# Kernel optimization log

Measured on AMD Instinct MI355X. Metric: run time of the kernel, lower is better.

The kernel has to match this reference:

```python
import jax, jax.numpy as jnp
from jax import lax
import numpy as np

B, C, FH, FW, H, V, L = 256, 512, 8, 16, 512, 64, 24


def setup_inputs() -> dict:
    key = jax.random.key(0)
    ks = jax.random.split(key, 32)
    s = 0.05
    n = lambda k, shp: jax.random.normal(k, shp, dtype=jnp.float32) * s
    return {
        "encoder_ftrs": jax.random.normal(ks[0], (B, C, FH, FW), dtype=jnp.float32),
        "sequences": jax.random.randint(ks[1], (B, L), 0, V),
        "test": 0,
        "embed_w": n(ks[2], (V, H)),
        "init_state": n(ks[3], (2, 1, H)),
        "attn_W_w": n(ks[4], (H, C)), "attn_W_b": jnp.zeros((H,), jnp.float32),
        "attn_U_w": n(ks[5], (H, H)), "attn_U_b": jnp.zeros((H,), jnp.float32),
        "attn_v_w": n(ks[6], (1, H)), "attn_v_b": jnp.zeros((1,), jnp.float32),
        "fc_w": n(ks[7], (H, C + H)), "fc_b": jnp.zeros((H,), jnp.float32),
        "cls_w": n(ks[8], (V, H)), "cls_b": jnp.zeros((V,), jnp.float32),
        "gru0_wih": n(ks[9], (3 * H, 2 * H)), "gru0_whh": n(ks[10], (3 * H, H)),
        "gru0_bih": jnp.zeros((3 * H,), jnp.float32), "gru0_bhh": jnp.zeros((3 * H,), jnp.float32),
        "gru1_wih": n(ks[11], (3 * H, H)), "gru1_whh": n(ks[12], (3 * H, H)),
        "gru1_bih": jnp.zeros((3 * H,), jnp.float32), "gru1_bhh": jnp.zeros((3 * H,), jnp.float32),
    }


def _gru_cell(x, h, wih, whh, bih, bhh):
    # PyTorch GRUCell: r,z gates then candidate n with r applied on hidden path
    gi = x @ wih.T + bih
    gh = h @ whh.T + bhh
    i_r, i_z, i_n = jnp.split(gi, 3, axis=-1)
    h_r, h_z, h_n = jnp.split(gh, 3, axis=-1)
    r = jax.nn.sigmoid(i_r + h_r)
    z = jax.nn.sigmoid(i_z + h_z)
    nact = jnp.tanh(i_n + r * h_n)
    return (1.0 - z) * nact + z * h


def reference(encoder_ftrs, sequences, test, embed_w, init_state,
              attn_W_w, attn_W_b, attn_U_w, attn_U_b, attn_v_w, attn_v_b,
              fc_w, fc_b, cls_w, cls_b,
              gru0_wih, gru0_whh, gru0_bih, gru0_bhh,
              gru1_wih, gru1_whh, gru1_bih, gru1_bhh):
    bsz = encoder_ftrs.shape[0]
    # [B, L_sp, C] encoder states
    states = encoder_ftrs.reshape(bsz, C, -1).transpose(0, 2, 1)
    # attn_W(states) is timestep-independent: precompute once (same math)
    Ws = states @ attn_W_w.T + attn_W_b  # [B, L_sp, H]

    def apply_attn(h_top):
        e = jax.nn.relu(Ws + (h_top @ attn_U_w.T + attn_U_b)[:, None, :])
        scores = e @ attn_v_w[0] + attn_v_b[0]          # [B, L_sp]
        a = jax.nn.softmax(scores, axis=-1)
        ctx = jnp.einsum('bl,blc->bc', a, states)        # [B, C]
        return ctx

    def out_proj(ctx, h_top):
        return jax.nn.relu(jnp.concatenate([ctx, h_top], axis=-1) @ fc_w.T + fc_b)

    xs = embed_w[sequences[:, :-1]]                      # [B, T, H]
    h0 = jnp.broadcast_to(init_state, (2, bsz, H))       # repeat over batch
    y0 = out_proj(apply_attn(h0[1]), h0[1])              # time_step == -1 (output dropped)

    def step(carry, x_t):
        h, y = carry
        h_l0 = _gru_cell(jnp.concatenate([y, x_t], axis=-1), h[0],
                         gru0_wih, gru0_whh, gru0_bih, gru0_bhh)
        h_l1 = _gru_cell(h_l0, h[1], gru1_wih, gru1_whh, gru1_bih, gru1_bhh)
        hn = jnp.stack([h_l0, h_l1], axis=0)
        yn = out_proj(apply_attn(h_l1), h_l1)
        return (hn, yn), yn

    _, ys = lax.scan(step, (h0, y0), xs.transpose(1, 0, 2))   # [T, B, H]
    logits = ys.transpose(1, 0, 2) @ cls_w.T + cls_b          # [B, T, V]

    labels = sequences[:, 1:]
    mask = (labels > 0).astype(logits.dtype)
    logp = jax.nn.log_softmax(logits, axis=-1)
    nll = -jnp.take_along_axis(logp, labels[..., None], axis=-1)[..., 0]
    loss = jnp.sum(nll * mask) / jnp.sum(mask)
    return loss
```

## Files before the change

kernel.cpp:

```cpp
#include <hip/hip_runtime.h>
#include <hip/hip_bf16.h>
#include <cstddef>

#define BB 256
#define CC 512
#define SS 128
#define HH 512
#define VV 64
#define LL 24

typedef unsigned short ush;
typedef __attribute__((ext_vector_type(8))) short short8;
typedef __attribute__((ext_vector_type(4))) float f32x4;

__device__ __forceinline__ float wave_sum(float v) {
#pragma unroll
    for (int off = 32; off > 0; off >>= 1) v += __shfl_xor(v, off);
    return v;
}
__device__ __forceinline__ float wave_max(float v) {
#pragma unroll
    for (int off = 32; off > 0; off >>= 1) v = fmaxf(v, __shfl_xor(v, off));
    return v;
}
__device__ __forceinline__ float sigm(float x) { return 1.0f / (1.0f + expf(-x)); }
__device__ __forceinline__ ush f2bf(float f) {
    unsigned u = __float_as_uint(f);
    u += 0x7FFFu + ((u >> 16) & 1u);
    return (ush)(u >> 16);
}
__device__ __forceinline__ float bf2f(ush b) {
    return __uint_as_float(((unsigned)b) << 16);
}
__device__ __forceinline__ unsigned pack2(float a, float b) {
    return (unsigned)f2bf(a) | ((unsigned)f2bf(b) << 16);
}

__global__ __launch_bounds__(256) void init_kernel(const float* __restrict__ init_state,
                                                   float* __restrict__ h0,
                                                   float* __restrict__ h1,
                                                   ush* __restrict__ h0b,
                                                   ush* __restrict__ h1b,
                                                   float* __restrict__ acc) {
    int idx = blockIdx.x * 256 + threadIdx.x;
    if (idx < BB * HH) {
        float a = init_state[idx & (HH - 1)];
        float b = init_state[HH + (idx & (HH - 1))];
        h0[idx] = a; h1[idx] = b;
        h0b[idx] = f2bf(a); h1b[idx] = f2bf(b);
    }
    if (idx < 2) acc[idx] = 0.0f;
}

__global__ __launch_bounds__(256) void conv_kernel(const float* __restrict__ src,
                                                   ush* __restrict__ dst, int n4) {
    int i = blockIdx.x * 256 + threadIdx.x;
    if (i < n4) {
        float4 v = ((const float4*)src)[i];
        uint2 o;
        o.x = pack2(v.x, v.y);
        o.y = pack2(v.z, v.w);
        ((uint2*)dst)[i] = o;
    }
}

__global__ __launch_bounds__(128) void gather_kernel(const float* __restrict__ embed_w,
                                                     const int* __restrict__ seq,
                                                     ush* __restrict__ xall) {
    int item = blockIdx.x;
    int t = item >> 8, m = item & 255;
    int row = seq[m * LL + t];
    float4 v = ((const float4*)(embed_w + (size_t)row * HH))[threadIdx.x];
    uint2 o;
    o.x = pack2(v.x, v.y);
    o.y = pack2(v.z, v.w);
    ((uint2*)(xall + (size_t)item * HH))[threadIdx.x] = o;
}

__global__ __launch_bounds__(256) void ws_mfma(const float* __restrict__ enc,
                                               const ush* __restrict__ Wb,
                                               const float* __restrict__ bias,
                                               ush* __restrict__ Ws_bf) {
    int tid = threadIdx.x;
    int wave = tid >> 6, lane = tid & 63;
    int quad = lane >> 4, l16 = lane & 15;
    int m0 = blockIdx.x * 256 + wave * 64;
    int n0 = blockIdx.y * 64;
    int b = m0 >> 7;
    int s_base = m0 & 127;
    const float* eb = enc + (size_t)b * CC * SS;
    const ush* wp = Wb + (size_t)(n0 + l16) * 512 + quad * 8;
    f32x4 acc[4][4];
#pragma unroll
    for (int f = 0; f < 4; f++)
#pragma unroll
        for (int s = 0; s < 4; s++) acc[f][s] = (f32x4){0.f, 0.f, 0.f, 0.f};
    for (int k0 = 0; k0 < 512; k0 += 32) {
        short8 af[4], bfr[4];
#pragma unroll
        for (int f = 0; f < 4; f++) {
            int s = s_base + f * 16 + l16;
#pragma unroll
            for (int j = 0; j < 8; j++) {
                float v = eb[(size_t)(k0 + quad * 8 + j) * SS + s];
                af[f][j] = (short)f2bf(v);
            }
        }
#pragma unroll
        for (int s = 0; s < 4; s++)
            bfr[s] = *(const short8*)(wp + (size_t)s * 16 * 512 + k0);
#pragma unroll
        for (int f = 0; f < 4; f++)
#pragma unroll
            for (int s = 0; s < 4; s++)
                acc[f][s] = __builtin_amdgcn_mfma_f32_16x16x32_bf16(af[f], bfr[s], acc[f][s], 0, 0, 0);
    }
#pragma unroll
    for (int f = 0; f < 4; f++)
#pragma unroll
        for (int s = 0; s < 4; s++)
#pragma unroll
            for (int r = 0; r < 4; r++) {
                int m = m0 + f * 16 + quad * 4 + r;
                int n = n0 + s * 16 + l16;
                Ws_bf[(size_t)m * HH + n] = f2bf(acc[f][s][r] + bias[n]);
            }
}

struct SkArgs {
    const ush* x[3];
    const ush* w[3];
    int wst[3];
};

__global__ __launch_bounds__(256) void mfma_gemm(SkArgs args, int N, int M,
                                                 float* __restrict__ P) {
    int tid = threadIdx.x;
    int wave = tid >> 6, lane = tid & 63;
    int quad = lane >> 4, l16 = lane & 15;
    int m0 = blockIdx.x * 64 + wave * 16;
    int n0 = blockIdx.y * 64;
    int z = blockIdx.z;
    const ush* X = args.x[z];
    const ush* W = args.w[z];
    int wst = args.wst[z];
    const ush* xp = X + (size_t)(m0 + l16) * 512 + quad * 8;
    const ush* wp = W + (size_t)(n0 + l16) * wst + quad * 8;
    f32x4 acc[4];
#pragma unroll
    for (int s = 0; s < 4; s++) acc[s] = (f32x4){0.f, 0.f, 0.f, 0.f};
    short8 a_c, b_c[4];
    a_c = *(const short8*)(xp);
#pragma unroll
    for (int s = 0; s < 4; s++) b_c[s] = *(const short8*)(wp + (size_t)s * 16 * wst);
#pragma unroll
    for (int ks = 0; ks < 16; ks++) {
        short8 a_n, b_n[4];
        if (ks < 15) {
            int k = (ks + 1) * 32;
            a_n = *(const short8*)(xp + k);
#pragma unroll
            for (int s = 0; s < 4; s++) b_n[s] = *(const short8*)(wp + (size_t)s * 16 * wst + k);
        }
#pragma unroll
        for (int s = 0; s < 4; s++)
            acc[s] = __builtin_amdgcn_mfma_f32_16x16x32_bf16(a_c, b_c[s], acc[s], 0, 0, 0);
        if (ks < 15) {
            a_c = a_n;
#pragma unroll
            for (int s = 0; s < 4; s++) b_c[s] = b_n[s];
        }
    }
#pragma unroll
    for (int s = 0; s < 4; s++)
#pragma unroll
        for (int r = 0; r < 4; r++) {
            int m = m0 + quad * 4 + r;
            int n = n0 + s * 16 + l16;
            P[((size_t)z * M + m) * N + n] = acc[s][r];
        }
}

template <int NSTEP>
__device__ __forceinline__ void segk(const ush* __restrict__ ap,
                                     const ush* __restrict__ bp,
                                     size_t wofs, f32x4& a0, f32x4& a1) {
    short8 as[4], bs0[4], bs1[4];
    constexpr int PRE = NSTEP < 4 ? NSTEP : 4;
#pragma unroll
    for (int i = 0; i < PRE; i++) {
        as[i]  = *(const short8*)(ap + 32 * i);
        bs0[i] = *(const short8*)(bp + 32 * i);
        bs1[i] = *(const short8*)(bp + wofs + 32 * i);
    }
#pragma unroll
    for (int i = 0; i < NSTEP; i++) {
        const int sl = i & 3;
        a0 = __builtin_amdgcn_mfma_f32_16x16x32_bf16(as[sl], bs0[sl], a0, 0, 0, 0);
        a1 = __builtin_amdgcn_mfma_f32_16x16x32_bf16(as[sl], bs1[sl], a1, 0, 0, 0);
        if (i + 4 < NSTEP) {
            as[sl]  = *(const short8*)(ap + 32 * (i + 4));
            bs0[sl] = *(const short8*)(bp + 32 * (i + 4));
            bs1[sl] = *(const short8*)(bp + wofs + 32 * (i + 4));
        }
    }
}

struct GruArgs {
    const ush* xs[4][3];
    const ush* wb[4][3];
    int wst[4][3];
    int nseg[4];
};

__global__ __launch_bounds__(256) void gru_fused(GruArgs A,
                                                 const float* __restrict__ h_prev,
                                                 const float* __restrict__ bih,
                                                 const float* __restrict__ bhh,
                                                 float* __restrict__ h_out,
                                                 ush* __restrict__ h_out_bf) {
    int tid = threadIdx.x;
    int wave = __builtin_amdgcn_readfirstlane(tid >> 6);
    int lane = tid & 63, quad = lane >> 4, l16 = lane & 15;
    int m0 = blockIdx.x * 16, n0 = blockIdx.y * 32;
    f32x4 acc0 = (f32x4){0.f, 0.f, 0.f, 0.f};
    f32x4 acc1 = (f32x4){0.f, 0.f, 0.f, 0.f};
    int ns = A.nseg[wave];
#pragma unroll
    for (int s = 0; s < 3; s++) {
        if (s < ns) {
            int wst = A.wst[wave][s];
            const ush* ap = A.xs[wave][s] + (size_t)(m0 + l16) * 512 + quad * 8;
            const ush* bp = A.wb[wave][s] + (size_t)(n0 + l16) * wst + quad * 8;
            segk<16>(ap, bp, (size_t)16 * wst, acc0, acc1);
        }
    }
    __shared__ float gbuf[4][16][32];
#pragma unroll
    for (int r = 0; r < 4; r++) {
        gbuf[wave][quad * 4 + r][l16]      = acc0[r];
        gbuf[wave][quad * 4 + r][16 + l16] = acc1[r];
    }
    __syncthreads();
#pragma unroll
    for (int e = 0; e < 2; e++) {
        int idx = e * 256 + tid;
        int mi = idx >> 5, ni = idx & 31;
        int n = n0 + ni;
        size_t off = (size_t)(m0 + mi) * HH + n;
        float r  = sigm(gbuf[0][mi][ni] + bih[n] + bhh[n]);
        float zf = sigm(gbuf[1][mi][ni] + bih[512 + n] + bhh[512 + n]);
        float na = tanhf(gbuf[2][mi][ni] + bih[1024 + n] +
                         r * (gbuf[3][mi][ni] + bhh[1024 + n]));
        float hp = h_prev[off];
        float ho = (1.0f - zf) * na + zf * hp;
        h_out[off] = ho;
        h_out_bf[off] = f2bf(ho);
    }
}

__global__ __launch_bounds__(256) void fc_fused(const ush* __restrict__ ctx,
                                                const ush* __restrict__ h,
                                                const ush* __restrict__ wFc,
                                                const float* __restrict__ bias,
                                                ush* __restrict__ y,
                                                ush* __restrict__ ys) {
    int tid = threadIdx.x;
    int wave = __builtin_amdgcn_readfirstlane(tid >> 6);
    int lane = tid & 63, quad = lane >> 4, l16 = lane & 15;
    int m0 = blockIdx.x * 16, n0 = blockIdx.y * 32;
    f32x4 acc0 = (f32x4){0.f, 0.f, 0.f, 0.f};
    f32x4 acc1 = (f32x4){0.f, 0.f, 0.f, 0.f};
    const ush* X = (wave < 2) ? ctx : h;
    int xco = (wave & 1) * 256;
    const ush* ap = X + (size_t)(m0 + l16) * 512 + xco + quad * 8;
    const ush* bp = wFc + (size_t)(n0 + l16) * 1024 + wave * 256 + quad * 8;
    segk<8>(ap, bp, (size_t)16 * 1024, acc0, acc1);
    __shared__ float gbuf[4][16][32];
#pragma unroll
    for (int r = 0; r < 4; r++) {
        gbuf[wave][quad * 4 + r][l16]      = acc0[r];
        gbuf[wave][quad * 4 + r][16 + l16] = acc1[r];
    }
    __syncthreads();
#pragma unroll
    for (int e = 0; e < 2; e++) {
        int idx = e * 256 + tid;
        int mi = idx >> 5, ni = idx & 31;
        int n = n0 + ni;
        float v = gbuf[0][mi][ni] + gbuf[1][mi][ni] + gbuf[2][mi][ni] +
                  gbuf[3][mi][ni] + bias[n];
        v = fmaxf(v, 0.0f);
        ush bb = f2bf(v);
        size_t off = (size_t)(m0 + mi) * HH + n;
        y[off] = bb;
        if (ys) ys[off] = bb;
    }
}

__global__ __launch_bounds__(256) void u_fused(const ush* __restrict__ h,
                                               const ush* __restrict__ wU,
                                               const float* __restrict__ Ub,
                                               float* __restrict__ Uo) {
    int tid = threadIdx.x;
    int wave = __builtin_amdgcn_readfirstlane(tid >> 6);
    int lane = tid & 63, quad = lane >> 4, l16 = lane & 15;
    int m0 = blockIdx.x * 16, n0 = blockIdx.y * 32;
    f32x4 acc0 = (f32x4){0.f, 0.f, 0.f, 0.f};
    f32x4 acc1 = (f32x4){0.f, 0.f, 0.f, 0.f};
    const ush* ap = h + (size_t)(m0 + l16) * 512 + wave * 128 + quad * 8;
    const ush* bp = wU + (size_t)(n0 + l16) * 512 + wave * 128 + quad * 8;
    segk<4>(ap, bp, (size_t)16 * 512, acc0, acc1);
    __shared__ float gbuf[4][16][32];
#pragma unroll
    for (int r = 0; r < 4; r++) {
        gbuf[wave][quad * 4 + r][l16]      = acc0[r];
        gbuf[wave][quad * 4 + r][16 + l16] = acc1[r];
    }
    __syncthreads();
#pragma unroll
    for (int e = 0; e < 2; e++) {
        int idx = e * 256 + tid;
        int mi = idx >> 5, ni = idx & 31;
        int n = n0 + ni;
        Uo[(size_t)(m0 + mi) * HH + n] = gbuf[0][mi][ni] + gbuf[1][mi][ni] +
                                         gbuf[2][mi][ni] + gbuf[3][mi][ni] + Ub[n];
    }
}

__global__ __launch_bounds__(256) void attn2(const float* __restrict__ u,
                                             const float* __restrict__ vw,
                                             const ush* __restrict__ Ws_bf,
                                             const ush* __restrict__ enc_bf,
                                             ush* __restrict__ ctx_bf) {
    int b = blockIdx.x;
    int tid = threadIdx.x;
    int wave = tid >> 6, lane = tid & 63;
    int hi = lane >> 4, li = lane & 15;
    __shared__ float a[SS];

    float ur[4][8], vr[4][8];
#pragma unroll
    for (int p = 0; p < 4; p++) {
        const float* up = u + (size_t)b * HH + p * 128 + li * 8;
        const float* vp = vw + p * 128 + li * 8;
        float4 u0 = *(const float4*)(up);
        float4 u1 = *(const float4*)(up + 4);
        float4 v0 = *(const float4*)(vp);
        float4 v1 = *(const float4*)(vp + 4);
        ur[p][0] = u0.x; ur[p][1] = u0.y; ur[p][2] = u0.z; ur[p][3] = u0.w;
        ur[p][4] = u1.x; ur[p][5] = u1.y; ur[p][6] = u1.z; ur[p][7] = u1.w;
        vr[p][0] = v0.x; vr[p][1] = v0.y; vr[p][2] = v0.z; vr[p][3] = v0.w;
        vr[p][4] = v1.x; vr[p][5] = v1.y; vr[p][6] = v1.z; vr[p][7] = v1.w;
    }
    const ush* wsb = Ws_bf + (size_t)b * SS * HH;
#pragma unroll
    for (int pass = 0; pass < 8; pass++) {
        int s = pass * 16 + wave * 4 + hi;
        float acc = 0.0f;
#pragma unroll
        for (int p = 0; p < 4; p++) {
            short8 rv = *(const short8*)(wsb + (size_t)s * HH + p * 128 + li * 8);
#pragma unroll
            for (int j = 0; j < 8; j++) {
                float e = bf2f((ush)rv[j]) + ur[p][j];
                acc += fmaxf(e, 0.0f) * vr[p][j];
            }
        }
#pragma unroll
        for (int off = 1; off < 16; off <<= 1) acc += __shfl_xor(acc, off);
        if (li == 0) a[s] = acc;
    }
    __syncthreads();
    if (wave == 0) {
        float s0v = a[lane], s1v = a[lane + 64];
        float m = wave_max(fmaxf(s0v, s1v));
        float e0 = expf(s0v - m), e1 = expf(s1v - m);
        float ssum = wave_sum(e0 + e1);
        float inv = 1.0f / ssum;
        a[lane] = e0 * inv;
        a[lane + 64] = e1 * inv;
    }
    __syncthreads();
    float ar[8];
#pragma unroll
    for (int j = 0; j < 8; j++) ar[j] = a[li * 8 + j];
    const ush* eb = enc_bf + (size_t)b * CC * SS;
#pragma unroll 4
    for (int pass = 0; pass < 32; pass++) {
        int c = pass * 16 + wave * 4 + hi;
        short8 ev = *(const short8*)(eb + (size_t)c * SS + li * 8);
        float acc = 0.0f;
#pragma unroll
        for (int j = 0; j < 8; j++) acc += bf2f((ush)ev[j]) * ar[j];
#pragma unroll
        for (int off = 1; off < 16; off <<= 1) acc += __shfl_xor(acc, off);
        if (li == 0) ctx_bf[(size_t)b * CC + c] = f2bf(acc);
    }
}

__global__ __launch_bounds__(64) void nll_kernel(const float* __restrict__ P,
                                                 const float* __restrict__ cls_b,
                                                 const int* __restrict__ seq,
                                                 float* __restrict__ acc) {
    int lane = threadIdx.x;
    float bias = cls_b[lane];
    float lsum = 0.0f, lcnt = 0.0f;
    for (int i = 0; i < 16; i++) {
        int item = blockIdx.x * 16 + i;
        int t = item >> 8, b = item & 255;
        float v = P[(size_t)item * VV + lane] + bias;
        float m = wave_max(v);
        float e = expf(v - m);
        float s = wave_sum(e);
        int label = seq[b * LL + t + 1];
        float vl = __shfl(v, label);
        if (lane == 0 && label > 0) {
            lsum += -(vl - m - logf(s));
            lcnt += 1.0f;
        }
    }
    if (lane == 0) {
        atomicAdd(&acc[0], lsum);
        atomicAdd(&acc[1], lcnt);
    }
}

__global__ void final_kernel(const float* __restrict__ acc, float* __restrict__ out) {
    if (threadIdx.x == 0) out[0] = acc[0] / acc[1];
}

extern "C" void kernel_launch(void* const* d_in, const int* in_sizes, int n_in,
                              void* d_out, int out_size, void* d_ws, size_t ws_size,
                              hipStream_t stream) {
    const float* enc        = (const float*)d_in[0];
    const int*   seq        = (const int*)d_in[1];
    const float* embed_w    = (const float*)d_in[3];
    const float* init_state = (const float*)d_in[4];
    const float* attn_W_w   = (const float*)d_in[5];
    const float* attn_W_b   = (const float*)d_in[6];
    const float* attn_U_w   = (const float*)d_in[7];
    const float* attn_U_b   = (const float*)d_in[8];
    const float* attn_v_w   = (const float*)d_in[9];
    const float* fc_w       = (const float*)d_in[11];
    const float* fc_b       = (const float*)d_in[12];
    const float* cls_w      = (const float*)d_in[13];
    const float* cls_b      = (const float*)d_in[14];
    const float* g0_wih     = (const float*)d_in[15];
    const float* g0_whh     = (const float*)d_in[16];
    const float* g0_bih     = (const float*)d_in[17];
    const float* g0_bhh     = (const float*)d_in[18];
    const float* g1_wih     = (const float*)d_in[19];
    const float* g1_whh     = (const float*)d_in[20];
    const float* g1_bih     = (const float*)d_in[21];
    const float* g1_bhh     = (const float*)d_in[22];
    float* out = (float*)d_out;

    float* ws = (float*)d_ws;
    size_t o = 0;
    ush* Ws_bf   = (ush*)(ws + o); o += (size_t)BB * SS * HH / 2;
    ush* enc_bf  = (ush*)(ws + o); o += (size_t)BB * CC * SS / 2;
    ush* ys_bf   = (ush*)(ws + o); o += (size_t)(LL - 1) * BB * HH / 2;
    ush* xall_bf = (ush*)(ws + o); o += (size_t)(LL - 1) * BB * HH / 2;
    ush* wWb  = (ush*)(ws + o); o += 262144 / 2;
    ush* wU   = (ush*)(ws + o); o += 262144 / 2;
    ush* wFc  = (ush*)(ws + o); o += 524288 / 2;
    ush* wCls = (ush*)(ws + o); o += 32768 / 2;
    ush* wG0i = (ush*)(ws + o); o += 1572864 / 2;
    ush* wG0h = (ush*)(ws + o); o += 786432 / 2;
    ush* wG1i = (ush*)(ws + o); o += 786432 / 2;
    ush* wG1h = (ush*)(ws + o); o += 786432 / 2;
    float* P    = ws + o; o += (size_t)3 * BB * 1536;
    float* Uo   = ws + o; o += (size_t)BB * HH;
    float* h0a  = ws + o; o += (size_t)BB * HH;
    float* h0b  = ws + o; o += (size_t)BB * HH;
    float* h1a  = ws + o; o += (size_t)BB * HH;
    float* h1b  = ws + o; o += (size_t)BB * HH;
    float* acc  = ws + o; o += 256;
    ush* h0a_bf = (ush*)(ws + o); o += (size_t)BB * HH / 2;
    ush* h0b_bf = (ush*)(ws + o); o += (size_t)BB * HH / 2;
    ush* h1a_bf = (ush*)(ws + o); o += (size_t)BB * HH / 2;
    ush* h1b_bf = (ush*)(ws + o); o += (size_t)BB * HH / 2;
    ush* y_bf   = (ush*)(ws + o); o += (size_t)BB * HH / 2;
    ush* ctx_bf = (ush*)(ws + o); o += (size_t)BB * CC / 2;
    float* Pcls = P;

    init_kernel<<<512, 256, 0, stream>>>(init_state, h0a, h1a, h0a_bf, h1a_bf, acc);
    conv_kernel<<<256, 256, 0, stream>>>(attn_W_w, wWb, 65536);
    conv_kernel<<<256, 256, 0, stream>>>(attn_U_w, wU, 65536);
    conv_kernel<<<512, 256, 0, stream>>>(fc_w, wFc, 131072);
    conv_kernel<<<32, 256, 0, stream>>>(cls_w, wCls, 8192);
    conv_kernel<<<1536, 256, 0, stream>>>(g0_wih, wG0i, 393216);
    conv_kernel<<<768, 256, 0, stream>>>(g0_whh, wG0h, 196608);
    conv_kernel<<<768, 256, 0, stream>>>(g1_wih, wG1i, 196608);
    conv_kernel<<<768, 256, 0, stream>>>(g1_whh, wG1h, 196608);
    conv_kernel<<<16384, 256, 0, stream>>>(enc, enc_bf, 4194304);
    gather_kernel<<<(LL - 1) * BB, 128, 0, stream>>>(embed_w, seq, xall_bf);
    ws_mfma<<<dim3(128, 8), 256, 0, stream>>>(enc, wWb, attn_W_b, Ws_bf);

    auto gru0_args = [&](const ush* y, const ush* x, const ush* h0) {
        GruArgs a{};
        a.xs[0][0] = y;  a.wb[0][0] = wG0i;                          a.wst[0][0] = 1024;
        a.xs[0][1] = x;  a.wb[0][1] = wG0i + 512;                    a.wst[0][1] = 1024;
        a.xs[0][2] = h0; a.wb[0][2] = wG0h;                          a.wst[0][2] = 512;
        a.nseg[0] = 3;
        a.xs[1][0] = y;  a.wb[1][0] = wG0i + (size_t)512 * 1024;        a.wst[1][0] = 1024;
        a.xs[1][1] = x;  a.wb[1][1] = wG0i + (size_t)512 * 1024 + 512;  a.wst[1][1] = 1024;
        a.xs[1][2] = h0; a.wb[1][2] = wG0h + (size_t)512 * 512;         a.wst[1][2] = 512;
        a.nseg[1] = 3;
        a.xs[2][0] = y;  a.wb[2][0] = wG0i + (size_t)1024 * 1024;       a.wst[2][0] = 1024;
        a.xs[2][1] = x;  a.wb[2][1] = wG0i + (size_t)1024 * 1024 + 512; a.wst[2][1] = 1024;
        a.nseg[2] = 2;
        a.xs[3][0] = h0; a.wb[3][0] = wG0h + (size_t)1024 * 512;        a.wst[3][0] = 512;
        a.nseg[3] = 1;
        return a;
    };
    auto gru1_args = [&](const ush* hl0, const ush* h1) {
        GruArgs a{};
        a.xs[0][0] = hl0; a.wb[0][0] = wG1i;                        a.wst[0][0] = 512;
        a.xs[0][1] = h1;  a.wb[0][1] = wG1h;                        a.wst[0][1] = 512;
        a.nseg[0] = 2;
        a.xs[1][0] = hl0; a.wb[1][0] = wG1i + (size_t)512 * 512;    a.wst[1][0] = 512;
        a.xs[1][1] = h1;  a.wb[1][1] = wG1h + (size_t)512 * 512;    a.wst[1][1] = 512;
        a.nseg[1] = 2;
        a.xs[2][0] = hl0; a.wb[2][0] = wG1i + (size_t)1024 * 512;   a.wst[2][0] = 512;
        a.nseg[2] = 1;
        a.xs[3][0] = h1;  a.wb[3][0] = wG1h + (size_t)1024 * 512;   a.wst[3][0] = 512;
        a.nseg[3] = 1;
        return a;
    };

    u_fused<<<dim3(16, 16), 256, 0, stream>>>(h1a_bf, wU, attn_U_b, Uo);
    attn2<<<BB, 256, 0, stream>>>(Uo, attn_v_w, Ws_bf, enc_bf, ctx_bf);
    fc_fused<<<dim3(16, 16), 256, 0, stream>>>(ctx_bf, h1a_bf, wFc, fc_b, y_bf, nullptr);

    float* h0_in = h0a; float* h0_out = h0b;
    float* h1_in = h1a; float* h1_out = h1b;
    ush* h0_in_bf = h0a_bf; ush* h0_out_bf = h0b_bf;
    ush* h1_in_bf = h1a_bf; ush* h1_out_bf = h1b_bf;
    for (int t = 0; t < LL - 1; t++) {
        gru_fused<<<dim3(16, 16), 256, 0, stream>>>(
            gru0_args(y_bf, xall_bf + (size_t)t * BB * HH, h0_in_bf),
            h0_in, g0_bih, g0_bhh, h0_out, h0_out_bf);
        gru_fused<<<dim3(16, 16), 256, 0, stream>>>(
            gru1_args(h0_out_bf, h1_in_bf),
            h1_in, g1_bih, g1_bhh, h1_out, h1_out_bf);
        u_fused<<<dim3(16, 16), 256, 0, stream>>>(h1_out_bf, wU, attn_U_b, Uo);
        attn2<<<BB, 256, 0, stream>>>(Uo, attn_v_w, Ws_bf, enc_bf, ctx_bf);
        fc_fused<<<dim3(16, 16), 256, 0, stream>>>(ctx_bf, h1_out_bf, wFc, fc_b,
                                                   y_bf, ys_bf + (size_t)t * BB * HH);
        float* tmp;
        tmp = h0_in; h0_in = h0_out; h0_out = tmp;
        tmp = h1_in; h1_in = h1_out; h1_out = tmp;
        ush* tb;
        tb = h0_in_bf; h0_in_bf = h0_out_bf; h0_out_bf = tb;
        tb = h1_in_bf; h1_in_bf = h1_out_bf; h1_out_bf = tb;
    }

    {
        SkArgs a{};
        a.x[0] = ys_bf; a.w[0] = wCls; a.wst[0] = 512;
        mfma_gemm<<<dim3(92, 1, 1), 256, 0, stream>>>(a, VV, 5888, Pcls);
    }
    nll_kernel<<<368, 64, 0, stream>>>(Pcls, cls_b, seq, acc);
    final_kernel<<<1, 1, 0, stream>>>(acc, out);
}
```

Baseline: 1.630 ms.

## Double waves per block in recurrent kernels, transpose encoder once, fuse classifier with NLL

The encoder features are converted once into a transposed bf16 [B,S,C] layout through an LDS tile. The Ws projection and the attention context pass now read that layout with contiguous vector loads. The GRU, U, FC and attention kernels move from 256 to 512 threads, with K split across 8 waves and reduced through shared memory, to cut the per-wave serial chain in each of the many small per-step launches. The classifier GEMM is fused with the log-softmax NLL into one kernel, removing the logits buffer and one launch. The extra shared-memory reductions and larger blocks add synchronisation and LDS traffic.

```diff
diff --git a/kernel.cpp b/kernel.cpp
--- a/kernel.cpp
+++ b/kernel.cpp
@@ -77,108 +77,91 @@
     ((uint2*)(xall + (size_t)item * HH))[threadIdx.x] = o;
 }
 
-__global__ __launch_bounds__(256) void ws_mfma(const float* __restrict__ enc,
-                                               const ush* __restrict__ Wb,
-                                               const float* __restrict__ bias,
-                                               ush* __restrict__ Ws_bf) {
+__global__ __launch_bounds__(256) void enc_conv(const float* __restrict__ enc,
+                                                ush* __restrict__ enc_t) {
+    int b = blockIdx.x, cg = blockIdx.y;
+    int c0 = cg * 128;
+    __shared__ ush tile[128][130];
+    const float* src = enc + ((size_t)b * 512 + c0) * 128;
+#pragma unroll
+    for (int i = 0; i < 16; i++) {
+        int lin = i * 256 + threadIdx.x;
+        int cl = lin >> 5, s4 = lin & 31;
+        float4 v = ((const float4*)(src + (size_t)cl * 128))[s4];
+        ush b0 = f2bf(v.x), b1 = f2bf(v.y), b2 = f2bf(v.z), b3 = f2bf(v.w);
+        tile[s4 * 4 + 0][cl] = b0;
+        tile[s4 * 4 + 1][cl] = b1;
+        tile[s4 * 4 + 2][cl] = b2;
+        tile[s4 * 4 + 3][cl] = b3;
+    }
+    __syncthreads();
+#pragma unroll
+    for (int i = 0; i < 16; i++) {
+        int lin = i * 256 + threadIdx.x;
+        int sl = lin >> 5, c4 = lin & 31;
+        ush a0 = tile[sl][c4 * 4 + 0], a1 = tile[sl][c4 * 4 + 1];
+        ush a2 = tile[sl][c4 * 4 + 2], a3 = tile[sl][c4 * 4 + 3];
+        uint2 o;
+        o.x = (unsigned)a0 | ((unsigned)a1 << 16);
+        o.y = (unsigned)a2 | ((unsigned)a3 << 16);
+        ((uint2*)(enc_t + ((size_t)b * 128 + sl) * 512 + c0))[c4] = o;
+    }
+}
+
+__global__ __launch_bounds__(256) void ws_v2(const ush* __restrict__ enc_t,
+                                             const ush* __restrict__ Wb,
+                                             const float* __restrict__ bias,
+                                             ush* __restrict__ Ws_bf) {
     int tid = threadIdx.x;
     int wave = tid >> 6, lane = tid & 63;
     int quad = lane >> 4, l16 = lane & 15;
-    int m0 = blockIdx.x * 256 + wave * 64;
-    int n0 = blockIdx.y * 64;
-    int b = m0 >> 7;
-    int s_base = m0 & 127;
-    const float* eb = enc + (size_t)b * CC * SS;
-    const ush* wp = Wb + (size_t)(n0 + l16) * 512 + quad * 8;
-    f32x4 acc[4][4];
-#pragma unroll
-    for (int f = 0; f < 4; f++)
-#pragma unroll
-        for (int s = 0; s < 4; s++) acc[f][s] = (f32x4){0.f, 0.f, 0.f, 0.f};
-    for (int k0 = 0; k0 < 512; k0 += 32) {
-        short8 af[4], bfr[4];
-#pragma unroll
-        for (int f = 0; f < 4; f++) {
-            int s = s_base + f * 16 + l16;
-#pragma unroll
-            for (int j = 0; j < 8; j++) {
-                float v = eb[(size_t)(k0 + quad * 8 + j) * SS + s];
-                af[f][j] = (short)f2bf(v);
-            }
-        }
-#pragma unroll
-        for (int s = 0; s < 4; s++)
-            bfr[s] = *(const short8*)(wp + (size_t)s * 16 * 512 + k0);
-#pragma unroll
-        for (int f = 0; f < 4; f++)
-#pragma unroll
-            for (int s = 0; s < 4; s++)
-                acc[f][s] = __builtin_amdgcn_mfma_f32_16x16x32_bf16(af[f], bfr[s], acc[f][s], 0, 0, 0);
-    }
-#pragma unroll
-    for (int f = 0; f < 4; f++)
-#pragma unroll
-        for (int s = 0; s < 4; s++)
+    int m0 = blockIdx.x * 128 + wave * 32;
+    int n0 = blockIdx.y * 128;
+    const ush* ap = enc_t + (size_t)(m0 + l16) * 512 + quad * 8;
+    const ush* bp = Wb + (size_t)(n0 + l16) * 512 + quad * 8;
+    f32x4 acc[2][8];
+#pragma unroll
+    for (int f = 0; f < 2; f++)
+#pragma unroll
+        for (int s = 0; s < 8; s++) acc[f][s] = (f32x4){0.f, 0.f, 0.f, 0.f};
+    short8 ac[2], bc[8], an[2], bn[8];
+    ac[0] = *(const short8*)(ap);
+    ac[1] = *(const short8*)(ap + (size_t)16 * 512);
+#pragma unroll
+    for (int s = 0; s < 8; s++) bc[s] = *(const short8*)(bp + (size_t)s * 16 * 512);
+#pragma unroll
+    for (int ks = 0; ks < 16; ks++) {
+        if (ks < 15) {
+            int k = (ks + 1) * 32;
+            an[0] = *(const short8*)(ap + k);
+            an[1] = *(const short8*)(ap + (size_t)16 * 512 + k);
+#pragma unroll
+            for (int s = 0; s < 8; s++)
+                bn[s] = *(const short8*)(bp + (size_t)s * 16 * 512 + k);
+        }
+#pragma unroll
+        for (int f = 0; f < 2; f++)
+#pragma unroll
+            for (int s = 0; s < 8; s++)
+                acc[f][s] = __builtin_amdgcn_mfma_f32_16x16x32_bf16(ac[f], bc[s], acc[f][s], 0, 0, 0);
+        if (ks < 15) {
+            ac[0] = an[0]; ac[1] = an[1];
+#pragma unroll
+            for (int s = 0; s < 8; s++) bc[s] = bn[s];
+        }
+    }
+#pragma unroll
+    for (int s = 0; s < 8; s++) {
+        int n = n0 + s * 16 + l16;
+        float bs = bias[n];
+#pragma unroll
+        for (int f = 0; f < 2; f++)
 #pragma unroll
             for (int r = 0; r < 4; r++) {
                 int m = m0 + f * 16 + quad * 4 + r;
-                int n = n0 + s * 16 + l16;
-                Ws_bf[(size_t)m * HH + n] = f2bf(acc[f][s][r] + bias[n]);
+                Ws_bf[(size_t)m * HH + n] = f2bf(acc[f][s][r] + bs);
             }
-}
-
-struct SkArgs {
-    const ush* x[3];
-    const ush* w[3];
-    int wst[3];
-};
-
-__global__ __launch_bounds__(256) void mfma_gemm(SkArgs args, int N, int M,
-                                                 float* __restrict__ P) {
-    int tid = threadIdx.x;
-    int wave = tid >> 6, lane = tid & 63;
-    int quad = lane >> 4, l16 = lane & 15;
-    int m0 = blockIdx.x * 64 + wave * 16;
-    int n0 = blockIdx.y * 64;
-    int z = blockIdx.z;
-    const ush* X = args.x[z];
-    const ush* W = args.w[z];
-    int wst = args.wst[z];
-    const ush* xp = X + (size_t)(m0 + l16) * 512 + quad * 8;
-    const ush* wp = W + (size_t)(n0 + l16) * wst + quad * 8;
-    f32x4 acc[4];
-#pragma unroll
-    for (int s = 0; s < 4; s++) acc[s] = (f32x4){0.f, 0.f, 0.f, 0.f};
-    short8 a_c, b_c[4];
-    a_c = *(const short8*)(xp);
-#pragma unroll
-    for (int s = 0; s < 4; s++) b_c[s] = *(const short8*)(wp + (size_t)s * 16 * wst);
-#pragma unroll
-    for (int ks = 0; ks < 16; ks++) {
-        short8 a_n, b_n[4];
-        if (ks < 15) {
-            int k = (ks + 1) * 32;
-            a_n = *(const short8*)(xp + k);
-#pragma unroll
-            for (int s = 0; s < 4; s++) b_n[s] = *(const short8*)(wp + (size_t)s * 16 * wst + k);
-        }
-#pragma unroll
-        for (int s = 0; s < 4; s++)
-            acc[s] = __builtin_amdgcn_mfma_f32_16x16x32_bf16(a_c, b_c[s], acc[s], 0, 0, 0);
-        if (ks < 15) {
-            a_c = a_n;
-#pragma unroll
-            for (int s = 0; s < 4; s++) b_c[s] = b_n[s];
-        }
-    }
-#pragma unroll
-    for (int s = 0; s < 4; s++)
-#pragma unroll
-        for (int r = 0; r < 4; r++) {
-            int m = m0 + quad * 4 + r;
-            int n = n0 + s * 16 + l16;
-            P[((size_t)z * M + m) * N + n] = acc[s][r];
-        }
+    }
 }
 
 template <int NSTEP>
@@ -207,13 +190,15 @@
 }
 
 struct GruArgs {
-    const ush* xs[4][3];
-    const ush* wb[4][3];
-    int wst[4][3];
-    int nseg[4];
+    const ush* xs[8][2];
+    const ush* wb[8][2];
+    int wst[8][2];
+    int nks[8][2];
+    int slot[8][2];
+    int zmask;
 };
 
-__global__ __launch_bounds__(256) void gru_fused(GruArgs A,
+__global__ __launch_bounds__(512) void gru_fused(GruArgs A,
                                                  const float* __restrict__ h_prev,
                                                  const float* __restrict__ bih,
                                                  const float* __restrict__ bhh,
@@ -223,35 +208,42 @@
     int wave = __builtin_amdgcn_readfirstlane(tid >> 6);
     int lane = tid & 63, quad = lane >> 4, l16 = lane & 15;
     int m0 = blockIdx.x * 16, n0 = blockIdx.y * 32;
-    f32x4 acc0 = (f32x4){0.f, 0.f, 0.f, 0.f};
-    f32x4 acc1 = (f32x4){0.f, 0.f, 0.f, 0.f};
-    int ns = A.nseg[wave];
-#pragma unroll
-    for (int s = 0; s < 3; s++) {
-        if (s < ns) {
-            int wst = A.wst[wave][s];
-            const ush* ap = A.xs[wave][s] + (size_t)(m0 + l16) * 512 + quad * 8;
-            const ush* bp = A.wb[wave][s] + (size_t)(n0 + l16) * wst + quad * 8;
-            segk<16>(ap, bp, (size_t)16 * wst, acc0, acc1);
-        }
-    }
-    __shared__ float gbuf[4][16][32];
-#pragma unroll
-    for (int r = 0; r < 4; r++) {
-        gbuf[wave][quad * 4 + r][l16]      = acc0[r];
-        gbuf[wave][quad * 4 + r][16 + l16] = acc1[r];
-    }
-    __syncthreads();
-#pragma unroll
+    __shared__ float gbuf[10][16][32];
+    if (A.zmask) {
+        int mi = tid >> 5, ni = tid & 31;
+#pragma unroll
+        for (int s = 0; s < 10; s++)
+            if ((A.zmask >> s) & 1) gbuf[s][mi][ni] = 0.0f;
+    }
     for (int e = 0; e < 2; e++) {
-        int idx = e * 256 + tid;
-        int mi = idx >> 5, ni = idx & 31;
+        int nks = A.nks[wave][e];
+        if (nks == 0) continue;
+        f32x4 a0 = (f32x4){0.f, 0.f, 0.f, 0.f};
+        f32x4 a1 = (f32x4){0.f, 0.f, 0.f, 0.f};
+        int wst = A.wst[wave][e];
+        const ush* ap = A.xs[wave][e] + (size_t)(m0 + l16) * 512 + quad * 8;
+        const ush* bp = A.wb[wave][e] + (size_t)(n0 + l16) * wst + quad * 8;
+        size_t wofs = (size_t)16 * wst;
+        if (nks == 16) segk<16>(ap, bp, wofs, a0, a1);
+        else           segk<8>(ap, bp, wofs, a0, a1);
+        int sl = A.slot[wave][e];
+#pragma unroll
+        for (int r = 0; r < 4; r++) {
+            gbuf[sl][quad * 4 + r][l16]      = a0[r];
+            gbuf[sl][quad * 4 + r][16 + l16] = a1[r];
+        }
+    }
+    __syncthreads();
+    {
+        int mi = tid >> 5, ni = tid & 31;
         int n = n0 + ni;
         size_t off = (size_t)(m0 + mi) * HH + n;
-        float r  = sigm(gbuf[0][mi][ni] + bih[n] + bhh[n]);
-        float zf = sigm(gbuf[1][mi][ni] + bih[512 + n] + bhh[512 + n]);
-        float na = tanhf(gbuf[2][mi][ni] + bih[1024 + n] +
-                         r * (gbuf[3][mi][ni] + bhh[1024 + n]));
+        float r  = sigm(gbuf[0][mi][ni] + gbuf[1][mi][ni] + gbuf[2][mi][ni] +
+                        bih[n] + bhh[n]);
+        float zf = sigm(gbuf[3][mi][ni] + gbuf[4][mi][ni] + gbuf[5][mi][ni] +
+                        bih[512 + n] + bhh[512 + n]);
+        float na = tanhf(gbuf[6][mi][ni] + gbuf[7][mi][ni] + bih[1024 + n] +
+                         r * (gbuf[8][mi][ni] + gbuf[9][mi][ni] + bhh[1024 + n]));
         float hp = h_prev[off];
         float ho = (1.0f - zf) * na + zf * hp;
         h_out[off] = ho;
@@ -259,7 +251,7 @@
     }
 }
 
-__global__ __launch_bounds__(256) void fc_fused(const ush* __restrict__ ctx,
+__global__ __launch_bounds__(512) void fc_fused(const ush* __restrict__ ctx,
                                                 const ush* __restrict__ h,
                                                 const ush* __restrict__ wFc,
                                                 const float* __restrict__ bias,
@@ -269,27 +261,26 @@
     int wave = __builtin_amdgcn_readfirstlane(tid >> 6);
     int lane = tid & 63, quad = lane >> 4, l16 = lane & 15;
     int m0 = blockIdx.x * 16, n0 = blockIdx.y * 32;
-    f32x4 acc0 = (f32x4){0.f, 0.f, 0.f, 0.f};
-    f32x4 acc1 = (f32x4){0.f, 0.f, 0.f, 0.f};
-    const ush* X = (wave < 2) ? ctx : h;
-    int xco = (wave & 1) * 256;
-    const ush* ap = X + (size_t)(m0 + l16) * 512 + xco + quad * 8;
-    const ush* bp = wFc + (size_t)(n0 + l16) * 1024 + wave * 256 + quad * 8;
-    segk<8>(ap, bp, (size_t)16 * 1024, acc0, acc1);
-    __shared__ float gbuf[4][16][32];
+    const ush* X = (wave < 4) ? ctx : h;
+    int q = wave & 3;
+    f32x4 a0 = (f32x4){0.f, 0.f, 0.f, 0.f};
+    f32x4 a1 = (f32x4){0.f, 0.f, 0.f, 0.f};
+    const ush* ap = X + (size_t)(m0 + l16) * 512 + q * 128 + quad * 8;
+    const ush* bp = wFc + (size_t)(n0 + l16) * 1024 + (wave >= 4 ? 512 : 0) + q * 128 + quad * 8;
+    segk<4>(ap, bp, (size_t)16 * 1024, a0, a1);
+    __shared__ float gbuf[8][16][32];
 #pragma unroll
     for (int r = 0; r < 4; r++) {
-        gbuf[wave][quad * 4 + r][l16]      = acc0[r];
-        gbuf[wave][quad * 4 + r][16 + l16] = acc1[r];
-    }
-    __syncthreads();
-#pragma unroll
-    for (int e = 0; e < 2; e++) {
-        int idx = e * 256 + tid;
-        int mi = idx >> 5, ni = idx & 31;
+        gbuf[wave][quad * 4 + r][l16]      = a0[r];
+        gbuf[wave][quad * 4 + r][16 + l16] = a1[r];
+    }
+    __syncthreads();
+    {
+        int mi = tid >> 5, ni = tid & 31;
         int n = n0 + ni;
-        float v = gbuf[0][mi][ni] + gbuf[1][mi][ni] + gbuf[2][mi][ni] +
-                  gbuf[3][mi][ni] + bias[n];
+        float v = bias[n];
+#pragma unroll
+        for (int w = 0; w < 8; w++) v += gbuf[w][mi][ni];
         v = fmaxf(v, 0.0f);
         ush bb = f2bf(v);
         size_t off = (size_t)(m0 + mi) * HH + n;
@@ -298,7 +289,7 @@
     }
 }
 
-__global__ __launch_bounds__(256) void u_fused(const ush* __restrict__ h,
+__global__ __launch_bounds__(512) void u_fused(const ush* __restrict__ h,
                                                const ush* __restrict__ wU,
                                                const float* __restrict__ Ub,
                                                float* __restrict__ Uo) {
@@ -306,38 +297,39 @@
     int wave = __builtin_amdgcn_readfirstlane(tid >> 6);
     int lane = tid & 63, quad = lane >> 4, l16 = lane & 15;
     int m0 = blockIdx.x * 16, n0 = blockIdx.y * 32;
-    f32x4 acc0 = (f32x4){0.f, 0.f, 0.f, 0.f};
-    f32x4 acc1 = (f32x4){0.f, 0.f, 0.f, 0.f};
-    const ush* ap = h + (size_t)(m0 + l16) * 512 + wave * 128 + quad * 8;
-    const ush* bp = wU + (size_t)(n0 + l16) * 512 + wave * 128 + quad * 8;
-    segk<4>(ap, bp, (size_t)16 * 512, acc0, acc1);
-    __shared__ float gbuf[4][16][32];
+    f32x4 a0 = (f32x4){0.f, 0.f, 0.f, 0.f};
+    f32x4 a1 = (f32x4){0.f, 0.f, 0.f, 0.f};
+    const ush* ap = h + (size_t)(m0 + l16) * 512 + wave * 64 + quad * 8;
+    const ush* bp = wU + (size_t)(n0 + l16) * 512 + wave * 64 + quad * 8;
+    segk<2>(ap, bp, (size_t)16 * 512, a0, a1);
+    __shared__ float gbuf[8][16][32];
 #pragma unroll
     for (int r = 0; r < 4; r++) {
-        gbuf[wave][quad * 4 + r][l16]      = acc0[r];
-        gbuf[wave][quad * 4 + r][16 + l16] = acc1[r];
-    }
-    __syncthreads();
-#pragma unroll
-    for (int e = 0; e < 2; e++) {
-        int idx = e * 256 + tid;
-        int mi = idx >> 5, ni = idx & 31;
+        gbuf[wave][quad * 4 + r][l16]      = a0[r];
+        gbuf[wave][quad * 4 + r][16 + l16] = a1[r];
+    }
+    __syncthreads();
+    {
+        int mi = tid >> 5, ni = tid & 31;
         int n = n0 + ni;
-        Uo[(size_t)(m0 + mi) * HH + n] = gbuf[0][mi][ni] + gbuf[1][mi][ni] +
-                                         gbuf[2][mi][ni] + gbuf[3][mi][ni] + Ub[n];
-    }
-}
-
-__global__ __launch_bounds__(256) void attn2(const float* __restrict__ u,
+        float v = Ub[n];
+#pragma unroll
+        for (int w = 0; w < 8; w++) v += gbuf[w][mi][ni];
+        Uo[(size_t)(m0 + mi) * HH + n] = v;
+    }
+}
+
+__global__ __launch_bounds__(512) void attn3(const float* __restrict__ u,
                                              const float* __restrict__ vw,
                                              const ush* __restrict__ Ws_bf,
-                                             const ush* __restrict__ enc_bf,
+                                             const ush* __restrict__ enc_t,
                                              ush* __restrict__ ctx_bf) {
     int b = blockIdx.x;
     int tid = threadIdx.x;
     int wave = tid >> 6, lane = tid & 63;
     int hi = lane >> 4, li = lane & 15;
     __shared__ float a[SS];
+    __shared__ float part[8][512];
 
     float ur[4][8], vr[4][8];
 #pragma unroll
@@ -355,8 +347,8 @@
     }
     const ush* wsb = Ws_bf + (size_t)b * SS * HH;
 #pragma unroll
-    for (int pass = 0; pass < 8; pass++) {
-        int s = pass * 16 + wave * 4 + hi;
+    for (int pass = 0; pass < 4; pass++) {
+        int s = pass * 32 + wave * 4 + hi;
         float acc = 0.0f;
 #pragma unroll
         for (int p = 0; p < 4; p++) {
@@ -382,47 +374,83 @@
         a[lane + 64] = e1 * inv;
     }
     __syncthreads();
-    float ar[8];
-#pragma unroll
-    for (int j = 0; j < 8; j++) ar[j] = a[li * 8 + j];
-    const ush* eb = enc_bf + (size_t)b * CC * SS;
-#pragma unroll 4
-    for (int pass = 0; pass < 32; pass++) {
-        int c = pass * 16 + wave * 4 + hi;
-        short8 ev = *(const short8*)(eb + (size_t)c * SS + li * 8);
-        float acc = 0.0f;
-#pragma unroll
-        for (int j = 0; j < 8; j++) acc += bf2f((ush)ev[j]) * ar[j];
-#pragma unroll
-        for (int off = 1; off < 16; off <<= 1) acc += __shfl_xor(acc, off);
-        if (li == 0) ctx_bf[(size_t)b * CC + c] = f2bf(acc);
-    }
-}
-
-__global__ __launch_bounds__(64) void nll_kernel(const float* __restrict__ P,
+    float c8[8];
+#pragma unroll
+    for (int j = 0; j < 8; j++) c8[j] = 0.0f;
+    const ush* ebt = enc_t + (size_t)b * SS * 512;
+#pragma unroll
+    for (int i = 0; i < 16; i++) {
+        int s = wave * 16 + i;
+        float as = a[s];
+        short8 ev = *(const short8*)(ebt + (size_t)s * 512 + lane * 8);
+#pragma unroll
+        for (int j = 0; j < 8; j++) c8[j] += as * bf2f((ush)ev[j]);
+    }
+    *(float4*)(&part[wave][lane * 8])     = (float4){c8[0], c8[1], c8[2], c8[3]};
+    *(float4*)(&part[wave][lane * 8 + 4]) = (float4){c8[4], c8[5], c8[6], c8[7]};
+    __syncthreads();
+    {
+        float sum = 0.0f;
+#pragma unroll
+        for (int w = 0; w < 8; w++) sum += part[w][tid];
+        ctx_bf[(size_t)b * CC + tid] = f2bf(sum);
+    }
+}
+
+__global__ __launch_bounds__(256) void cls_fused(const ush* __restrict__ ys,
+                                                 const ush* __restrict__ wCls,
                                                  const float* __restrict__ cls_b,
                                                  const int* __restrict__ seq,
                                                  float* __restrict__ acc) {
-    int lane = threadIdx.x;
-    float bias = cls_b[lane];
+    int tid = threadIdx.x;
+    int wave = tid >> 6, lane = tid & 63;
+    int quad = lane >> 4, l16 = lane & 15;
+    int m0 = blockIdx.x * 16;
+    f32x4 a4[4];
+#pragma unroll
+    for (int s = 0; s < 4; s++) a4[s] = (f32x4){0.f, 0.f, 0.f, 0.f};
+    const ush* ap = ys + (size_t)(m0 + l16) * 512 + wave * 128 + quad * 8;
+    const ush* bp = wCls + (size_t)l16 * 512 + wave * 128 + quad * 8;
+#pragma unroll
+    for (int ks = 0; ks < 4; ks++) {
+        short8 av = *(const short8*)(ap + ks * 32);
+#pragma unroll
+        for (int s = 0; s < 4; s++) {
+            short8 bv = *(const short8*)(bp + (size_t)s * 16 * 512 + ks * 32);
+            a4[s] = __builtin_amdgcn_mfma_f32_16x16x32_bf16(av, bv, a4[s], 0, 0, 0);
+        }
+    }
+    __shared__ float gbuf[4][16][64];
+    __shared__ float red[8];
+#pragma unroll
+    for (int s = 0; s < 4; s++)
+#pragma unroll
+        for (int r = 0; r < 4; r++)
+            gbuf[wave][quad * 4 + r][s * 16 + l16] = a4[s][r];
+    __syncthreads();
     float lsum = 0.0f, lcnt = 0.0f;
-    for (int i = 0; i < 16; i++) {
-        int item = blockIdx.x * 16 + i;
+#pragma unroll
+    for (int ii = 0; ii < 4; ii++) {
+        int mi = wave * 4 + ii;
+        int item = m0 + mi;
         int t = item >> 8, b = item & 255;
-        float v = P[(size_t)item * VV + lane] + bias;
-        float m = wave_max(v);
-        float e = expf(v - m);
-        float s = wave_sum(e);
+        float v = gbuf[0][mi][lane] + gbuf[1][mi][lane] + gbuf[2][mi][lane] +
+                  gbuf[3][mi][lane] + cls_b[lane];
+        float mx = wave_max(v);
+        float e = expf(v - mx);
+        float ssum = wave_sum(e);
         int label = seq[b * LL + t + 1];
         float vl = __shfl(v, label);
-        if (lane == 0 && label > 0) {
-            lsum += -(vl - m - logf(s));
+        if (label > 0) {
+            lsum += -(vl - mx - logf(ssum));
             lcnt += 1.0f;
         }
     }
-    if (lane == 0) {
-        atomicAdd(&acc[0], lsum);
-        atomicAdd(&acc[1], lcnt);
+    if (lane == 0) { red[wave] = lsum; red[4 + wave] = lcnt; }
+    __syncthreads();
+    if (tid == 0) {
+        atomicAdd(&acc[0], red[0] + red[1] + red[2] + red[3]);
+        atomicAdd(&acc[1], red[4] + red[5] + red[6] + red[7]);
     }
 }
 
@@ -459,7 +487,7 @@
     float* ws = (float*)d_ws;
     size_t o = 0;
     ush* Ws_bf   = (ush*)(ws + o); o += (size_t)BB * SS * HH / 2;
-    ush* enc_bf  = (ush*)(ws + o); o += (size_t)BB * CC * SS / 2;
+    ush* enc_t   = (ush*)(ws + o); o += (size_t)BB * CC * SS / 2;
     ush* ys_bf   = (ush*)(ws + o); o += (size_t)(LL - 1) * BB * HH / 2;
     ush* xall_bf = (ush*)(ws + o); o += (size_t)(LL - 1) * BB * HH / 2;
     ush* wWb  = (ush*)(ws + o); o += 262144 / 2;
@@ -470,7 +498,6 @@
     ush* wG0h = (ush*)(ws + o); o += 786432 / 2;
     ush* wG1i = (ush*)(ws + o); o += 786432 / 2;
     ush* wG1h = (ush*)(ws + o); o += 786432 / 2;
-    float* P    = ws + o; o += (size_t)3 * BB * 1536;
     float* Uo   = ws + o; o += (size_t)BB * HH;
     float* h0a  = ws + o; o += (size_t)BB * HH;
     float* h0b  = ws + o; o += (size_t)BB * HH;
@@ -483,7 +510,6 @@
     ush* h1b_bf = (ush*)(ws + o); o += (size_t)BB * HH / 2;
     ush* y_bf   = (ush*)(ws + o); o += (size_t)BB * HH / 2;
     ush* ctx_bf = (ush*)(ws + o); o += (size_t)BB * CC / 2;
-    float* Pcls = P;
 
     init_kernel<<<512, 256, 0, stream>>>(init_state, h0a, h1a, h0a_bf, h1a_bf, acc);
     conv_kernel<<<256, 256, 0, stream>>>(attn_W_w, wWb, 65536);
@@ -494,60 +520,62 @@
     conv_kernel<<<768, 256, 0, stream>>>(g0_whh, wG0h, 196608);
     conv_kernel<<<768, 256, 0, stream>>>(g1_wih, wG1i, 196608);
     conv_kernel<<<768, 256, 0, stream>>>(g1_whh, wG1h, 196608);
-    conv_kernel<<<16384, 256, 0, stream>>>(enc, enc_bf, 4194304);
+    enc_conv<<<dim3(256, 4), 256, 0, stream>>>(enc, enc_t);
     gather_kernel<<<(LL - 1) * BB, 128, 0, stream>>>(embed_w, seq, xall_bf);
-    ws_mfma<<<dim3(128, 8), 256, 0, stream>>>(enc, wWb, attn_W_b, Ws_bf);
-
+    ws_v2<<<dim3(256, 4), 256, 0, stream>>>(enc_t, wWb, attn_W_b, Ws_bf);
+
+    auto setw = [](GruArgs& a, int w, int e, const ush* xs, const ush* wb,
+                   int wst, int nks, int slot) {
+        a.xs[w][e] = xs; a.wb[w][e] = wb; a.wst[w][e] = wst;
+        a.nks[w][e] = nks; a.slot[w][e] = slot;
+    };
     auto gru0_args = [&](const ush* y, const ush* x, const ush* h0) {
         GruArgs a{};
-        a.xs[0][0] = y;  a.wb[0][0] = wG0i;                          a.wst[0][0] = 1024;
-        a.xs[0][1] = x;  a.wb[0][1] = wG0i + 512;                    a.wst[0][1] = 1024;
-        a.xs[0][2] = h0; a.wb[0][2] = wG0h;                          a.wst[0][2] = 512;
-        a.nseg[0] = 3;
-        a.xs[1][0] = y;  a.wb[1][0] = wG0i + (size_t)512 * 1024;        a.wst[1][0] = 1024;
-        a.xs[1][1] = x;  a.wb[1][1] = wG0i + (size_t)512 * 1024 + 512;  a.wst[1][1] = 1024;
-        a.xs[1][2] = h0; a.wb[1][2] = wG0h + (size_t)512 * 512;         a.wst[1][2] = 512;
-        a.nseg[1] = 3;
-        a.xs[2][0] = y;  a.wb[2][0] = wG0i + (size_t)1024 * 1024;       a.wst[2][0] = 1024;
-        a.xs[2][1] = x;  a.wb[2][1] = wG0i + (size_t)1024 * 1024 + 512; a.wst[2][1] = 1024;
-        a.nseg[2] = 2;
-        a.xs[3][0] = h0; a.wb[3][0] = wG0h + (size_t)1024 * 512;        a.wst[3][0] = 512;
-        a.nseg[3] = 1;
+        setw(a, 0, 0, y,        wG0i,                             1024, 16, 0);
+        setw(a, 1, 0, x,        wG0i + 512,                       1024, 16, 1);
+        setw(a, 2, 0, h0,       wG0h,                              512, 16, 2);
+        setw(a, 3, 0, y,        wG0i + (size_t)512 * 1024,        1024, 16, 3);
+        setw(a, 4, 0, x,        wG0i + (size_t)512 * 1024 + 512,  1024, 16, 4);
+        setw(a, 5, 0, h0,       wG0h + (size_t)512 * 512,          512, 16, 5);
+        setw(a, 6, 0, y,        wG0i + (size_t)1024 * 1024,       1024, 16, 6);
+        setw(a, 7, 0, x,        wG0i + (size_t)1024 * 1024 + 512, 1024, 16, 7);
+        setw(a, 6, 1, h0,       wG0h + (size_t)1024 * 512,         512,  8, 8);
+        setw(a, 7, 1, h0 + 256, wG0h + (size_t)1024 * 512 + 256,   512,  8, 9);
+        a.zmask = 0;
         return a;
     };
     auto gru1_args = [&](const ush* hl0, const ush* h1) {
         GruArgs a{};
-        a.xs[0][0] = hl0; a.wb[0][0] = wG1i;                        a.wst[0][0] = 512;
-        a.xs[0][1] = h1;  a.wb[0][1] = wG1h;                        a.wst[0][1] = 512;
-        a.nseg[0] = 2;
-        a.xs[1][0] = hl0; a.wb[1][0] = wG1i + (size_t)512 * 512;    a.wst[1][0] = 512;
-        a.xs[1][1] = h1;  a.wb[1][1] = wG1h + (size_t)512 * 512;    a.wst[1][1] = 512;
-        a.nseg[1] = 2;
-        a.xs[2][0] = hl0; a.wb[2][0] = wG1i + (size_t)1024 * 512;   a.wst[2][0] = 512;
-        a.nseg[2] = 1;
-        a.xs[3][0] = h1;  a.wb[3][0] = wG1h + (size_t)1024 * 512;   a.wst[3][0] = 512;
-        a.nseg[3] = 1;
+        setw(a, 0, 0, hl0,       wG1i,                             512, 16, 0);
+        setw(a, 1, 0, h1,        wG1h,                             512, 16, 1);
+        setw(a, 2, 0, hl0,       wG1i + (size_t)512 * 512,         512, 16, 3);
+        setw(a, 3, 0, h1,        wG1h + (size_t)512 * 512,         512, 16, 4);
+        setw(a, 4, 0, hl0,       wG1i + (size_t)1024 * 512,        512,  8, 6);
+        setw(a, 5, 0, hl0 + 256, wG1i + (size_t)1024 * 512 + 256,  512,  8, 7);
+        setw(a, 6, 0, h1,        wG1h + (size_t)1024 * 512,        512,  8, 8);
+        setw(a, 7, 0, h1 + 256,  wG1h + (size_t)1024 * 512 + 256,  512,  8, 9);
+        a.zmask = (1 << 2) | (1 << 5);
         return a;
     };
 
-    u_fused<<<dim3(16, 16), 256, 0, stream>>>(h1a_bf, wU, attn_U_b, Uo);
-    attn2<<<BB, 256, 0, stream>>>(Uo, attn_v_w, Ws_bf, enc_bf, ctx_bf);
-    fc_fused<<<dim3(16, 16), 256, 0, stream>>>(ctx_bf, h1a_bf, wFc, fc_b, y_bf, nullptr);
+    u_fused<<<dim3(16, 16), 512, 0, stream>>>(h1a_bf, wU, attn_U_b, Uo);
+    attn3<<<BB, 512, 0, stream>>>(Uo, attn_v_w, Ws_bf, enc_t, ctx_bf);
+    fc_fused<<<dim3(16, 16), 512, 0, stream>>>(ctx_bf, h1a_bf, wFc, fc_b, y_bf, nullptr);
 
     float* h0_in = h0a; float* h0_out = h0b;
     float* h1_in = h1a; float* h1_out = h1b;
     ush* h0_in_bf = h0a_bf; ush* h0_out_bf = h0b_bf;
     ush* h1_in_bf = h1a_bf; ush* h1_out_bf = h1b_bf;
     for (int t = 0; t < LL - 1; t++) {
-        gru_fused<<<dim3(16, 16), 256, 0, stream>>>(
+        gru_fused<<<dim3(16, 16), 512, 0, stream>>>(
             gru0_args(y_bf, xall_bf + (size_t)t * BB * HH, h0_in_bf),
             h0_in, g0_bih, g0_bhh, h0_out, h0_out_bf);
-        gru_fused<<<dim3(16, 16), 256, 0, stream>>>(
+        gru_fused<<<dim3(16, 16), 512, 0, stream>>>(
             gru1_args(h0_out_bf, h1_in_bf),
             h1_in, g1_bih, g1_bhh, h1_out, h1_out_bf);
-        u_fused<<<dim3(16, 16), 256, 0, stream>>>(h1_out_bf, wU, attn_U_b, Uo);
-        attn2<<<BB, 256, 0, stream>>>(Uo, attn_v_w, Ws_bf, enc_bf, ctx_bf);
-        fc_fused<<<dim3(16, 16), 256, 0, stream>>>(ctx_bf, h1_out_bf, wFc, fc_b,
+        u_fused<<<dim3(16, 16), 512, 0, stream>>>(h1_out_bf, wU, attn_U_b, Uo);
+        attn3<<<BB, 512, 0, stream>>>(Uo, attn_v_w, Ws_bf, enc_t, ctx_bf);
+        fc_fused<<<dim3(16, 16), 512, 0, stream>>>(ctx_bf, h1_out_bf, wFc, fc_b,
                                                    y_bf, ys_bf + (size_t)t * BB * HH);
         float* tmp;
         tmp = h0_in; h0_in = h0_out; h0_out = tmp;
@@ -557,11 +585,6 @@
         tb = h1_in_bf; h1_in_bf = h1_out_bf; h1_out_bf = tb;
     }
 
-    {
-        SkArgs a{};
-        a.x[0] = ys_bf; a.w[0] = wCls; a.wst[0] = 512;
-        mfma_gemm<<<dim3(92, 1, 1), 256, 0, stream>>>(a, VV, 5888, Pcls);
-    }
-    nll_kernel<<<368, 64, 0, stream>>>(Pcls, cls_b, seq, acc);
+    cls_fused<<<368, 256, 0, stream>>>(ys_bf, wCls, cls_b, seq, acc);
     final_kernel<<<1, 1, 0, stream>>>(acc, out);
 }
```

Result: faster. 1.395 ms (-14.4%).
